# Kernel tuning notes

Measured on AMD Instinct MI355X. Metric: run time of the kernel, lower is better.

Reference implementation:

```python
import jax, jax.numpy as jnp
import numpy as np

B, K, D, H = 4, 2048, 768, 12
HD = D // H
NEG = -1e30  # stands in for -inf in the additive mask


def setup_inputs() -> dict:
    key = jax.random.key(0)
    ks = jax.random.split(key, 11)
    s = 1.0 / np.sqrt(D)
    inp = {
        "x": jax.random.normal(ks[0], (B, K, D), jnp.float32),
        "is_context": jax.random.randint(ks[1], (B, K), 0, 2) > 0,
        "Wq": jax.random.normal(ks[2], (D, D), jnp.float32) * s,
        "bq": jax.random.normal(ks[3], (D,), jnp.float32) * 0.01,
        "Wk": jax.random.normal(ks[4], (D, D), jnp.float32) * s,
        "bk": jax.random.normal(ks[5], (D,), jnp.float32) * 0.01,
        "Wv": jax.random.normal(ks[6], (D, D), jnp.float32) * s,
        "bv": jax.random.normal(ks[7], (D,), jnp.float32) * 0.01,
        "Wo": jax.random.normal(ks[8], (D, D), jnp.float32) * s,
        "bo": jax.random.normal(ks[9], (D,), jnp.float32) * 0.01,
    }
    return inp


def reference(x, is_context, Wq, bq, Wk, bk, Wv, bv, Wo, bo):
    b, k_len, d = x.shape
    scale = 1.0 / jnp.sqrt(jnp.asarray(HD, x.dtype))
    # torch nn.Linear: y = x @ W.T + b
    q = (x @ Wq.T + bq).reshape(b, k_len, H, HD).transpose(0, 2, 1, 3)  # [B,H,K,hd]
    kk = (x @ Wk.T + bk).reshape(b, k_len, H, HD).transpose(0, 2, 1, 3)
    v = (x @ Wv.T + bv).reshape(b, k_len, H, HD).transpose(0, 2, 1, 3)

    ctx = is_context  # [B,K] bool
    # allowed[b,i,j]: context rows attend only to context cols; target rows attend to all
    allowed = (ctx[:, :, None] & ctx[:, None, :]) | (~ctx)[:, :, None]  # [B,K,K]

    scores = jnp.einsum("bhqd,bhkd->bhqk", q, kk) * scale  # [B,H,K,K]
    scores = jnp.where(allowed[:, None, :, :], scores, NEG)
    attn = jax.nn.softmax(scores, axis=-1)
    out = jnp.einsum("bhqk,bhkd->bhqd", attn, v)  # [B,H,K,hd]
    out = out.transpose(0, 2, 1, 3).reshape(b, k_len, d)
    return out @ Wo.T + bo
```

## Files before the change

### kernel.cpp

```cpp
#include <hip/hip_runtime.h>
#include <hip/hip_bf16.h>

constexpr int BATCH = 4;
constexpr int SEQ   = 2048;
constexpr int DIM   = 768;
constexpr int NH    = 12;
constexpr int HDIM  = 64;

typedef __attribute__((ext_vector_type(8))) short bf16x8;
typedef __attribute__((ext_vector_type(4))) float f32x4;
typedef __attribute__((ext_vector_type(4))) short s16x4;

__device__ inline short f2bf(float f) {
    union { float f; unsigned u; } v; v.f = f;
    unsigned r = (v.u + 0x7fff + ((v.u >> 16) & 1)) >> 16;
    return (short)r;
}

__device__ inline unsigned pack_bf16x2(float a, float b) {
    union { __hip_bfloat162 h; unsigned u; } c;
    c.h = __float22bfloat162_rn(make_float2(a, b));
    return c.u;
}

__device__ inline float fast_exp2(float x) {
#if __has_builtin(__builtin_amdgcn_exp2f)
    return __builtin_amdgcn_exp2f(x);
#else
    return __expf(x * 0.6931471805599453f);
#endif
}

__device__ inline void gld16(const short* g, short* l) {
    __builtin_amdgcn_global_load_lds(
        (const __attribute__((address_space(1))) void*)g,
        (__attribute__((address_space(3))) void*)l, 16, 0, 0);
}

__device__ inline bool ctx_at(const void* p, bool isU8, int idx) {
    return isU8 ? (((const unsigned char*)p)[idx] != 0)
                : (((const int*)p)[idx] != 0);
}

__global__ __launch_bounds__(256) void prep_kernel(
    const float* __restrict__ x,  const float* __restrict__ Wq,
    const float* __restrict__ Wk, const float* __restrict__ Wv,
    const float* __restrict__ Wo,
    short* __restrict__ xb,  short* __restrict__ Wqb,
    short* __restrict__ Wkb, short* __restrict__ Wvb,
    short* __restrict__ Wob,
    const unsigned char* __restrict__ ctxm, int ctxbytes, int* __restrict__ flag) {
    const int blk = blockIdx.x;
    constexpr int XBLK = (BATCH * SEQ * DIM / 4) / 256;
    constexpr int WBLK = (DIM * DIM / 4) / 256;

    if (blk == XBLK + 4 * WBLK) {
        __shared__ int cnt;
        if (threadIdx.x == 0) cnt = 0;
        __syncthreads();
        int local = 0;
        for (int i = threadIdx.x; i < ctxbytes; i += 256)
            if ((i & 3) != 0 && ctxm[i] != 0) local++;
        atomicAdd(&cnt, local);
        __syncthreads();
        if (threadIdx.x == 0) *flag = (cnt > 0) ? 1 : 0;
        return;
    }

    const float* src; short* dst; int i;
    if (blk < XBLK) {
        src = x; dst = xb;
        i = blk * 256 + threadIdx.x;
    } else {
        const int r = blk - XBLK;
        const int w = r / WBLK;
        src = (w == 0) ? Wq : (w == 1) ? Wk : (w == 2) ? Wv : Wo;
        dst = (w == 0) ? Wqb : (w == 1) ? Wkb : (w == 2) ? Wvb : Wob;
        i = (r - w * WBLK) * 256 + threadIdx.x;
    }
    float4 v = ((const float4*)src)[i];
    s16x4 o;
    o.x = f2bf(v.x); o.y = f2bf(v.y); o.z = f2bf(v.z); o.w = f2bf(v.w);
    ((s16x4*)dst)[i] = o;
}

template <bool BF16OUT, bool VT>
__global__ __launch_bounds__(256) void gemm_mfma(
    const short* __restrict__ A,
    const short* __restrict__ W0, const float* __restrict__ bias0, void* __restrict__ C0,
    const short* __restrict__ W1, const float* __restrict__ bias1, void* __restrict__ C1,
    const short* __restrict__ W2, const float* __restrict__ bias2, void* __restrict__ C2,
    float scale0) {
    constexpr int N  = DIM;
    constexpr int Kd = DIM;

    const short* W; const float* bias; void* C; float scale;
    if (blockIdx.z == 0)      { W = W0; bias = bias0; C = C0; scale = scale0; }
    else if (blockIdx.z == 1) { W = W1; bias = bias1; C = C1; scale = 1.f; }
    else                      { W = W2; bias = bias2; C = C2; scale = 1.f; }

    const int tid  = threadIdx.x;
    const int wave = tid >> 6;
    const int lane = tid & 63;
    const int quad = lane >> 4;
    const int l16  = lane & 15;
    const int wm   = wave & 1;
    const int wn   = wave >> 1;
    const int m0   = blockIdx.y * 128;
    const int n0   = blockIdx.x * 128;

    __shared__ short As[128 * 32];
    __shared__ short Bs[128 * 32];

    const int srow = tid >> 2;
    const int skq  = tid & 3;
    const short* Ag = A + (size_t)(m0 + srow) * Kd + skq * 8;
    const short* Wg = W + (size_t)(n0 + srow) * Kd + skq * 8;
    short* AsP = As + srow * 32 + skq * 8;
    short* BsP = Bs + srow * 32 + skq * 8;

    f32x4 acc[4][4] = {};

    for (int kt = 0; kt < Kd; kt += 32) {
        __syncthreads();
        gld16(Ag + kt,                AsP);
        gld16(Ag + kt + 64 * Kd,      AsP + 64 * 32);
        gld16(Wg + kt,                BsP);
        gld16(Wg + kt + 64 * Kd,      BsP + 64 * 32);
        __syncthreads();

        bf16x8 af[4], bfr[4];
#pragma unroll
        for (int mt = 0; mt < 4; ++mt)
            af[mt] = *(const bf16x8*)&As[(wm * 64 + mt * 16 + l16) * 32 + quad * 8];
#pragma unroll
        for (int nt = 0; nt < 4; ++nt)
            bfr[nt] = *(const bf16x8*)&Bs[(wn * 64 + nt * 16 + l16) * 32 + quad * 8];
#pragma unroll
        for (int mt = 0; mt < 4; ++mt)
#pragma unroll
            for (int nt = 0; nt < 4; ++nt)
                acc[mt][nt] = __builtin_amdgcn_mfma_f32_16x16x32_bf16(
                    af[mt], bfr[nt], acc[mt][nt], 0, 0, 0);
    }

    float bv[4];
#pragma unroll
    for (int nt = 0; nt < 4; ++nt) bv[nt] = bias[n0 + wn * 64 + nt * 16 + l16];

    if (VT && blockIdx.z == 2) {
        const int tok0 = m0 + wm * 64;
        const int bb   = tok0 >> 11;
        const int tt   = (tok0 & (SEQ - 1)) >> 6;
        short* Vt = (short*)C;
#pragma unroll
        for (int mt = 0; mt < 4; ++mt) {
            const int p_base = ((mt & 2) << 4) +
                               ((mt & 1) ? (((quad ^ 2) << 3) + 4) : (quad << 3));
#pragma unroll
            for (int nt = 0; nt < 4; ++nt) {
                const int n    = n0 + wn * 64 + nt * 16 + l16;
                const int hh   = n >> 6;
                const int dcol = n & 63;
                s16x4 o;
#pragma unroll
                for (int reg = 0; reg < 4; ++reg)
                    o[reg] = f2bf(acc[mt][nt][reg] + bv[nt]);
                *(s16x4*)(Vt + ((size_t)((bb * NH + hh) * HDIM + dcol)) * SEQ
                          + tt * 64 + p_base) = o;
            }
        }
        return;
    }

#pragma unroll
    for (int mt = 0; mt < 4; ++mt)
#pragma unroll
        for (int nt = 0; nt < 4; ++nt)
#pragma unroll
            for (int reg = 0; reg < 4; ++reg) {
                const int m = m0 + wm * 64 + mt * 16 + quad * 4 + reg;
                const int n = n0 + wn * 64 + nt * 16 + l16;
                const float v = (acc[mt][nt][reg] + bv[nt]) * scale;
                if (BF16OUT) ((short*)C)[(size_t)m * N + n] = f2bf(v);
                else         ((float*)C)[(size_t)m * N + n] = v;
            }
}

__global__ __launch_bounds__(256, 3) void attn_mfma9(
    const short* __restrict__ Qb, const short* __restrict__ Kb,
    const short* __restrict__ Vtg, const void* __restrict__ ctxp,
    const int* __restrict__ flagp, short* __restrict__ Ob) {
    const int swz  = (blockIdx.x & 7) * 96 + (blockIdx.x >> 3);
    const int qc   = swz & 15;
    const int h    = (swz >> 4) % NH;
    const int b    = swz / (16 * NH);
    const int q0   = qc * 128;
    const int tid  = threadIdx.x;
    const int wave = tid >> 6;
    const int lane = tid & 63;
    const int quad = lane >> 4;
    const int l16  = lane & 15;
    const bool isU8 = (*flagp != 0);

    __shared__ short Ks[3][64 * 64];
    __shared__ short Vs[3][64 * 64];

    const short* Kg = Kb + (size_t)b * SEQ * DIM + h * HDIM;
    const short* Vg = Vtg + (size_t)(b * NH + h) * HDIM * SEQ;

    const int r0 = tid >> 3;
    const int j0 = (tid & 7) ^ (r0 & 7);
    const int sw = l16 & 7;

    bf16x8 qf[2][2];
#pragma unroll
    for (int rg = 0; rg < 2; ++rg) {
        const short* qp = Qb + (size_t)(b * SEQ + q0 + wave * 32 + rg * 16 + l16) * DIM
                        + h * HDIM + quad * 8;
        qf[rg][0] = *(const bf16x8*)qp;
        qf[rg][1] = *(const bf16x8*)(qp + 32);
    }

    unsigned nmb[2];
#pragma unroll
    for (int rg = 0; rg < 2; ++rg)
        nmb[rg] = ctx_at(ctxp, isU8,
            b * SEQ + q0 + wave * 32 + rg * 16 + l16) ? 0u : 0xFFFFFFFFu;

    constexpr int NT = SEQ / 64;
    unsigned kbits = 0;
#pragma unroll
    for (int t = 0; t < NT; ++t)
        kbits |= (ctx_at(ctxp, isU8, b * SEQ + t * 64 + lane) ? 1u : 0u) << t;

    bf16x8 ones;
#pragma unroll
    for (int i = 0; i < 8; ++i) ones[i] = (short)0x3F80;

    f32x4 accl[2] = {};
    f32x4 acc[2][4] = {};

    auto stage = [&](int t) {
        short* KD = Ks[t % 3];
        short* VD = Vs[t % 3];
        const int kn = t * 64;
        gld16(Kg + (size_t)(kn + r0) * DIM + j0 * 8,      KD + tid * 8);
        gld16(Kg + (size_t)(kn + r0 + 32) * DIM + j0 * 8, KD + (tid + 256) * 8);
        gld16(Vg + (size_t)r0 * SEQ + kn + j0 * 8,        VD + tid * 8);
        gld16(Vg + (size_t)(r0 + 32) * SEQ + kn + j0 * 8, VD + (tid + 256) * 8);
    };

    auto qk = [&](const short* BK, f32x4 (&sd)[4][2]) {
#pragma unroll
        for (int g = 0; g < 4; ++g) { sd[g][0] = (f32x4){}; sd[g][1] = (f32x4){}; }
        __builtin_amdgcn_s_setprio(1);
#pragma unroll
        for (int ks = 0; ks < 2; ++ks) {
            bf16x8 kf[4];
#pragma unroll
            for (int g = 0; g < 4; ++g)
                kf[g] = *(const bf16x8*)
                    &BK[(g * 16 + l16) * 64 + (((ks * 4 + quad) ^ sw)) * 8];
#pragma unroll
            for (int g = 0; g < 4; ++g) {
                sd[g][0] = __builtin_amdgcn_mfma_f32_16x16x32_bf16(kf[g], qf[0][ks], sd[g][0], 0, 0, 0);
                sd[g][1] = __builtin_amdgcn_mfma_f32_16x16x32_bf16(kf[g], qf[1][ks], sd[g][1], 0, 0, 0);
            }
        }
        __builtin_amdgcn_s_setprio(0);
    };

    auto sm_pv = [&](f32x4 (&sp)[4][2], int t, const short* BV) {
        const unsigned long long kmask = __ballot((kbits >> t) & 1u);
        unsigned mw[2][4];
#pragma unroll
        for (int ks = 0; ks < 2; ++ks)
#pragma unroll
            for (int w = 0; w < 4; ++w) {
                const int base = 32 * ks + ((w >> 1) & 1) * 16 + quad * 4 + (w & 1) * 2;
                const unsigned two = (unsigned)(kmask >> base) & 3u;
                mw[ks][w] = ((two & 1u) ? 0x0000FFFFu : 0u) |
                            ((two & 2u) ? 0xFFFF0000u : 0u);
            }

        bf16x8 pa[2][2];
#pragma unroll
        for (int rg = 0; rg < 2; ++rg) {
            const unsigned nm = nmb[rg];
#pragma unroll
            for (int ks = 0; ks < 2; ++ks) {
                const int g0 = 2 * ks, g1 = 2 * ks + 1;
                const float e0 = fast_exp2(sp[g0][rg][0]);
                const float e1 = fast_exp2(sp[g0][rg][1]);
                const float e2 = fast_exp2(sp[g0][rg][2]);
                const float e3 = fast_exp2(sp[g0][rg][3]);
                const float e4 = fast_exp2(sp[g1][rg][0]);
                const float e5 = fast_exp2(sp[g1][rg][1]);
                const float e6 = fast_exp2(sp[g1][rg][2]);
                const float e7 = fast_exp2(sp[g1][rg][3]);
                const unsigned wA0 = pack_bf16x2(e0, e1) & (nm | mw[ks][0]);
                const unsigned wA1 = pack_bf16x2(e2, e3) & (nm | mw[ks][1]);
                const unsigned wB0 = pack_bf16x2(e4, e5) & (nm | mw[ks][2]);
                const unsigned wB1 = pack_bf16x2(e6, e7) & (nm | mw[ks][3]);
                const unsigned pB0 = (unsigned)__shfl((int)wB0, lane ^ 32);
                const unsigned pB1 = (unsigned)__shfl((int)wB1, lane ^ 32);
                union { bf16x8 v; unsigned u[4]; } tb;
                tb.u[0] = wA0; tb.u[1] = wA1; tb.u[2] = pB0; tb.u[3] = pB1;
                pa[rg][ks] = tb.v;
            }
        }

        __builtin_amdgcn_s_setprio(1);
#pragma unroll
        for (int ks = 0; ks < 2; ++ks) {
            accl[0] = __builtin_amdgcn_mfma_f32_16x16x32_bf16(pa[0][ks], ones, accl[0], 0, 0, 0);
            accl[1] = __builtin_amdgcn_mfma_f32_16x16x32_bf16(pa[1][ks], ones, accl[1], 0, 0, 0);
#pragma unroll
            for (int dt = 0; dt < 4; ++dt) {
                bf16x8 vf = *(const bf16x8*)
                    &BV[(dt * 16 + l16) * 64 + (((ks * 4 + quad) ^ sw)) * 8];
                acc[0][dt] = __builtin_amdgcn_mfma_f32_16x16x32_bf16(pa[0][ks], vf, acc[0][dt], 0, 0, 0);
                acc[1][dt] = __builtin_amdgcn_mfma_f32_16x16x32_bf16(pa[1][ks], vf, acc[1][dt], 0, 0, 0);
            }
        }
        __builtin_amdgcn_s_setprio(0);
    };

    f32x4 sA[4][2], sB[4][2];

    stage(0);
    stage(1);
    asm volatile("s_waitcnt vmcnt(4)" ::: "memory");
    __builtin_amdgcn_sched_barrier(0);
    __builtin_amdgcn_s_barrier();
    __builtin_amdgcn_sched_barrier(0);
    qk(Ks[0], sA);

    auto body = [&](int t, f32x4 (&prev)[4][2], f32x4 (&next)[4][2]) {
        __builtin_amdgcn_s_barrier();
        __builtin_amdgcn_sched_barrier(0);
        if (t + 2 < NT) stage(t + 2);
        if (t < NT - 2) { asm volatile("s_waitcnt vmcnt(4)" ::: "memory"); }
        else            { asm volatile("s_waitcnt vmcnt(0)" ::: "memory"); }
        __builtin_amdgcn_sched_barrier(0);
        __builtin_amdgcn_s_barrier();
        __builtin_amdgcn_sched_barrier(0);
        if (t + 1 < NT) qk(Ks[(t + 1) % 3], next);
        sm_pv(prev, t, Vs[t % 3]);
    };

    for (int t2 = 0; t2 < NT; t2 += 2) {
        body(t2,     sA, sB);
        body(t2 + 1, sB, sA);
    }

    float inv[2][4];
#pragma unroll
    for (int rg = 0; rg < 2; ++rg)
#pragma unroll
        for (int reg = 0; reg < 4; ++reg)
            inv[rg][reg] = 1.f / accl[rg][reg];

#pragma unroll
    for (int rg = 0; rg < 2; ++rg)
#pragma unroll
        for (int dt = 0; dt < 4; ++dt)
#pragma unroll
            for (int reg = 0; reg < 4; ++reg) {
                const int q = q0 + wave * 32 + rg * 16 + quad * 4 + reg;
                Ob[(size_t)(b * SEQ + q) * DIM + h * HDIM + dt * 16 + l16] =
                    f2bf(acc[rg][dt][reg] * inv[rg][reg]);
            }
}

extern "C" void kernel_launch(void* const* d_in, const int* in_sizes, int n_in,
                              void* d_out, int out_size, void* d_ws, size_t ws_size,
                              hipStream_t stream) {
    const float* x   = (const float*)d_in[0];
    const void*  ctx = d_in[1];
    const float* Wq  = (const float*)d_in[2];
    const float* bq  = (const float*)d_in[3];
    const float* Wk  = (const float*)d_in[4];
    const float* bk  = (const float*)d_in[5];
    const float* Wv  = (const float*)d_in[6];
    const float* bv  = (const float*)d_in[7];
    const float* Wo  = (const float*)d_in[8];
    const float* bo  = (const float*)d_in[9];
    float* out = (float*)d_out;

    char* ws = (char*)d_ws;
    int* flag = (int*)ws;
    const size_t bufbf = (size_t)BATCH * SEQ * DIM * sizeof(short);
    const size_t wbuf  = (size_t)DIM * DIM * sizeof(short);
    short* xb  = (short*)(ws + 256);
    short* Qb  = (short*)(ws + 256 + bufbf);
    short* Kb  = (short*)(ws + 256 + 2 * bufbf);
    short* Ab  = (short*)(ws + 256 + 4 * bufbf);
    short* Vtg = (short*)(ws + 256 + 5 * bufbf);
    short* Wqb = (short*)(ws + 256 + 6 * bufbf);
    short* Wkb = (short*)(ws + 256 + 6 * bufbf + wbuf);
    short* Wvb = (short*)(ws + 256 + 6 * bufbf + 2 * wbuf);
    short* Wob = (short*)(ws + 256 + 6 * bufbf + 3 * wbuf);

    constexpr int XBLK = (BATCH * SEQ * DIM / 4) / 256;
    constexpr int WBLK = (DIM * DIM / 4) / 256;
    prep_kernel<<<XBLK + 4 * WBLK + 1, 256, 0, stream>>>(
        x, Wq, Wk, Wv, Wo, xb, Wqb, Wkb, Wvb, Wob,
        (const unsigned char*)ctx, BATCH * SEQ, flag);

    dim3 gQKV(DIM / 128, (BATCH * SEQ) / 128, 3);
    gemm_mfma<true, true><<<gQKV, 256, 0, stream>>>(
        xb, Wqb, bq, Qb, Wkb, bk, Kb, Wvb, bv, Vtg, 0.125f * 1.4426950408889634f);

    attn_mfma9<<<dim3(SEQ / 128 * NH * BATCH, 1, 1), 256, 0, stream>>>(
        Qb, Kb, Vtg, ctx, flag, Ab);

    dim3 gOut(DIM / 128, (BATCH * SEQ) / 128, 1);
    gemm_mfma<false, false><<<gOut, 256, 0, stream>>>(
        Ab, Wob, bo, out, Wob, bo, out, Wob, bo, out, 1.f);
}
```

Before: 262.8 us.

## Split attention key range across two wave groups with LDS reduction

Doubles the attention workgroup to 512 threads. Two groups of four waves each process alternating 64-key tiles of the same 128-query block, and each round stages a pair of K/V tiles into double-buffered LDS. The per-wave partial outputs and row sums are combined through LDS at the end before normalization. This replaces the triple-buffered software pipeline, where QK of the next tile overlapped softmax/PV of the current one, with plain __syncthreads double buffering. The aim is more in-flight waves per block, at the cost of a reduction step and possibly less intra-wave overlap.

Measured after the change: 290.4 us. 10.5% more time.

```diff
diff --git a/kernel.cpp b/kernel.cpp
--- a/kernel.cpp
+++ b/kernel.cpp
@@ -187,7 +187,7 @@
             }
 }
 
-__global__ __launch_bounds__(256, 3) void attn_mfma9(
+__global__ __launch_bounds__(512, 4) void attn_mfma10(
     const short* __restrict__ Qb, const short* __restrict__ Kb,
     const short* __restrict__ Vtg, const void* __restrict__ ctxp,
     const int* __restrict__ flagp, short* __restrict__ Ob) {
@@ -198,13 +198,16 @@
     const int q0   = qc * 128;
     const int tid  = threadIdx.x;
     const int wave = tid >> 6;
+    const int wg   = wave & 3;
+    const int p    = wave >> 2;
     const int lane = tid & 63;
     const int quad = lane >> 4;
     const int l16  = lane & 15;
     const bool isU8 = (*flagp != 0);
 
-    __shared__ short Ks[3][64 * 64];
-    __shared__ short Vs[3][64 * 64];
+    __shared__ short Sm[32768];
+    auto KP = [&](int buf, int sub) { return Sm + (buf * 2 + sub) * 4096; };
+    auto VP = [&](int buf, int sub) { return Sm + 16384 + (buf * 2 + sub) * 4096; };
 
     const short* Kg = Kb + (size_t)b * SEQ * DIM + h * HDIM;
     const short* Vg = Vtg + (size_t)(b * NH + h) * HDIM * SEQ;
@@ -216,7 +219,7 @@
     bf16x8 qf[2][2];
 #pragma unroll
     for (int rg = 0; rg < 2; ++rg) {
-        const short* qp = Qb + (size_t)(b * SEQ + q0 + wave * 32 + rg * 16 + l16) * DIM
+        const short* qp = Qb + (size_t)(b * SEQ + q0 + wg * 32 + rg * 16 + l16) * DIM
                         + h * HDIM + quad * 8;
         qf[rg][0] = *(const bf16x8*)qp;
         qf[rg][1] = *(const bf16x8*)(qp + 32);
@@ -226,9 +229,10 @@
 #pragma unroll
     for (int rg = 0; rg < 2; ++rg)
         nmb[rg] = ctx_at(ctxp, isU8,
-            b * SEQ + q0 + wave * 32 + rg * 16 + l16) ? 0u : 0xFFFFFFFFu;
+            b * SEQ + q0 + wg * 32 + rg * 16 + l16) ? 0u : 0xFFFFFFFFu;
 
     constexpr int NT = SEQ / 64;
+    constexpr int NR = NT / 2;
     unsigned kbits = 0;
 #pragma unroll
     for (int t = 0; t < NT; ++t)
@@ -241,19 +245,27 @@
     f32x4 accl[2] = {};
     f32x4 acc[2][4] = {};
 
-    auto stage = [&](int t) {
-        short* KD = Ks[t % 3];
-        short* VD = Vs[t % 3];
-        const int kn = t * 64;
-        gld16(Kg + (size_t)(kn + r0) * DIM + j0 * 8,      KD + tid * 8);
-        gld16(Kg + (size_t)(kn + r0 + 32) * DIM + j0 * 8, KD + (tid + 256) * 8);
-        gld16(Vg + (size_t)r0 * SEQ + kn + j0 * 8,        VD + tid * 8);
-        gld16(Vg + (size_t)(r0 + 32) * SEQ + kn + j0 * 8, VD + (tid + 256) * 8);
+    auto stageRound = [&](int rr) {
+        const int buf = rr & 1;
+#pragma unroll
+        for (int sub = 0; sub < 2; ++sub) {
+            const int tp = 2 * rr + sub;
+            gld16(Kg + (size_t)(tp * 64 + r0) * DIM + j0 * 8, KP(buf, sub) + tid * 8);
+            gld16(Vg + (size_t)r0 * SEQ + tp * 64 + j0 * 8,   VP(buf, sub) + tid * 8);
+        }
     };
 
-    auto qk = [&](const short* BK, f32x4 (&sd)[4][2]) {
-#pragma unroll
-        for (int g = 0; g < 4; ++g) { sd[g][0] = (f32x4){}; sd[g][1] = (f32x4){}; }
+    stageRound(0);
+
+    for (int r = 0; r < NR; ++r) {
+        __syncthreads();
+        if (r + 1 < NR) stageRound(r + 1);
+
+        const int tt = 2 * r + p;
+        const short* BK = KP(r & 1, p);
+        const short* BV = VP(r & 1, p);
+
+        f32x4 s4[4][2] = {};
         __builtin_amdgcn_s_setprio(1);
 #pragma unroll
         for (int ks = 0; ks < 2; ++ks) {
@@ -264,15 +276,13 @@
                     &BK[(g * 16 + l16) * 64 + (((ks * 4 + quad) ^ sw)) * 8];
 #pragma unroll
             for (int g = 0; g < 4; ++g) {
-                sd[g][0] = __builtin_amdgcn_mfma_f32_16x16x32_bf16(kf[g], qf[0][ks], sd[g][0], 0, 0, 0);
-                sd[g][1] = __builtin_amdgcn_mfma_f32_16x16x32_bf16(kf[g], qf[1][ks], sd[g][1], 0, 0, 0);
+                s4[g][0] = __builtin_amdgcn_mfma_f32_16x16x32_bf16(kf[g], qf[0][ks], s4[g][0], 0, 0, 0);
+                s4[g][1] = __builtin_amdgcn_mfma_f32_16x16x32_bf16(kf[g], qf[1][ks], s4[g][1], 0, 0, 0);
             }
         }
         __builtin_amdgcn_s_setprio(0);
-    };
-
-    auto sm_pv = [&](f32x4 (&sp)[4][2], int t, const short* BV) {
-        const unsigned long long kmask = __ballot((kbits >> t) & 1u);
+
+        const unsigned long long kmask = __ballot((kbits >> tt) & 1u);
         unsigned mw[2][4];
 #pragma unroll
         for (int ks = 0; ks < 2; ++ks)
@@ -291,14 +301,14 @@
 #pragma unroll
             for (int ks = 0; ks < 2; ++ks) {
                 const int g0 = 2 * ks, g1 = 2 * ks + 1;
-                const float e0 = fast_exp2(sp[g0][rg][0]);
-                const float e1 = fast_exp2(sp[g0][rg][1]);
-                const float e2 = fast_exp2(sp[g0][rg][2]);
-                const float e3 = fast_exp2(sp[g0][rg][3]);
-                const float e4 = fast_exp2(sp[g1][rg][0]);
-                const float e5 = fast_exp2(sp[g1][rg][1]);
-                const float e6 = fast_exp2(sp[g1][rg][2]);
-                const float e7 = fast_exp2(sp[g1][rg][3]);
+                const float e0 = fast_exp2(s4[g0][rg][0]);
+                const float e1 = fast_exp2(s4[g0][rg][1]);
+                const float e2 = fast_exp2(s4[g0][rg][2]);
+                const float e3 = fast_exp2(s4[g0][rg][3]);
+                const float e4 = fast_exp2(s4[g1][rg][0]);
+                const float e5 = fast_exp2(s4[g1][rg][1]);
+                const float e6 = fast_exp2(s4[g1][rg][2]);
+                const float e7 = fast_exp2(s4[g1][rg][3]);
                 const unsigned wA0 = pack_bf16x2(e0, e1) & (nm | mw[ks][0]);
                 const unsigned wA1 = pack_bf16x2(e2, e3) & (nm | mw[ks][1]);
                 const unsigned wB0 = pack_bf16x2(e4, e5) & (nm | mw[ks][2]);
@@ -325,53 +335,37 @@
             }
         }
         __builtin_amdgcn_s_setprio(0);
-    };
-
-    f32x4 sA[4][2], sB[4][2];
-
-    stage(0);
-    stage(1);
-    asm volatile("s_waitcnt vmcnt(4)" ::: "memory");
-    __builtin_amdgcn_sched_barrier(0);
-    __builtin_amdgcn_s_barrier();
-    __builtin_amdgcn_sched_barrier(0);
-    qk(Ks[0], sA);
-
-    auto body = [&](int t, f32x4 (&prev)[4][2], f32x4 (&next)[4][2]) {
-        __builtin_amdgcn_s_barrier();
-        __builtin_amdgcn_sched_barrier(0);
-        if (t + 2 < NT) stage(t + 2);
-        if (t < NT - 2) { asm volatile("s_waitcnt vmcnt(4)" ::: "memory"); }
-        else            { asm volatile("s_waitcnt vmcnt(0)" ::: "memory"); }
-        __builtin_amdgcn_sched_barrier(0);
-        __builtin_amdgcn_s_barrier();
-        __builtin_amdgcn_sched_barrier(0);
-        if (t + 1 < NT) qk(Ks[(t + 1) % 3], next);
-        sm_pv(prev, t, Vs[t % 3]);
-    };
-
-    for (int t2 = 0; t2 < NT; t2 += 2) {
-        body(t2,     sA, sB);
-        body(t2 + 1, sB, sA);
-    }
-
-    float inv[2][4];
-#pragma unroll
-    for (int rg = 0; rg < 2; ++rg)
-#pragma unroll
-        for (int reg = 0; reg < 4; ++reg)
-            inv[rg][reg] = 1.f / accl[rg][reg];
-
-#pragma unroll
-    for (int rg = 0; rg < 2; ++rg)
-#pragma unroll
-        for (int dt = 0; dt < 4; ++dt)
-#pragma unroll
-            for (int reg = 0; reg < 4; ++reg) {
-                const int q = q0 + wave * 32 + rg * 16 + quad * 4 + reg;
-                Ob[(size_t)(b * SEQ + q) * DIM + h * HDIM + dt * 16 + l16] =
-                    f2bf(acc[rg][dt][reg] * inv[rg][reg]);
-            }
+    }
+
+    __syncthreads();
+    float* Sp = (float*)Sm;
+    const int slotW = (wave * 64 + lane) * 21;
+    const int ro = p ^ 1;
+#pragma unroll
+    for (int dt = 0; dt < 4; ++dt)
+#pragma unroll
+        for (int i = 0; i < 4; ++i)
+            Sp[slotW + dt * 4 + i] = acc[ro][dt][i];
+#pragma unroll
+    for (int i = 0; i < 4; ++i) Sp[slotW + 16 + i] = accl[ro][i];
+    __syncthreads();
+
+    const int slotR = ((wave ^ 4) * 64 + lane) * 21;
+    const int rs = p;
+    float inv[4];
+#pragma unroll
+    for (int i = 0; i < 4; ++i)
+        inv[i] = 1.f / (accl[rs][i] + Sp[slotR + 16 + i]);
+
+#pragma unroll
+    for (int dt = 0; dt < 4; ++dt)
+#pragma unroll
+        for (int reg = 0; reg < 4; ++reg) {
+            const int q = q0 + wg * 32 + rs * 16 + quad * 4 + reg;
+            const float o = acc[rs][dt][reg] + Sp[slotR + dt * 4 + reg];
+            Ob[(size_t)(b * SEQ + q) * DIM + h * HDIM + dt * 16 + l16] =
+                f2bf(o * inv[reg]);
+        }
 }
 
 extern "C" void kernel_launch(void* const* d_in, const int* in_sizes, int n_in,
@@ -413,7 +407,7 @@
     gemm_mfma<true, true><<<gQKV, 256, 0, stream>>>(
         xb, Wqb, bq, Qb, Wkb, bk, Kb, Wvb, bv, Vtg, 0.125f * 1.4426950408889634f);
 
-    attn_mfma9<<<dim3(SEQ / 128 * NH * BATCH, 1, 1), 256, 0, stream>>>(
+    attn_mfma10<<<dim3(SEQ / 128 * NH * BATCH, 1, 1), 512, 0, stream>>>(
         Qb, Kb, Vtg, ctx, flag, Ab);
 
     dim3 gOut(DIM / 128, (BATCH * SEQ) / 128, 1);
```
